# Kernel optimization log

Measured on AMD Instinct MI355X. Metric: run time of the kernel, lower is better.

The kernel has to match this reference:

```python
import jax, jax.numpy as jnp
import numpy as np

B, N, E = 32, 2048, 65536
SLOPE = 0.01  # torch LeakyReLU default

def _lrelu(x):
    return jax.nn.leaky_relu(x, SLOPE)

def setup_inputs() -> dict:
    key = jax.random.key(0)
    ks = jax.random.split(key, 32)
    def w(k, shape):
        return jax.random.normal(k, shape, dtype=jnp.float32) * 0.1
    inp = {}
    inp['vertices'] = jax.random.normal(ks[0], (B, N, 11), dtype=jnp.float32)
    inp['edges'] = jax.random.randint(ks[1], (2, E), 0, N, dtype=jnp.int32)
    # x/y/th pairwise feature extractors: Conv2d(1,8,kernel=(1,2)) == linear 2->8
    inp['Wx'], inp['bx'] = w(ks[2], (8, 2)), w(ks[3], (8,))
    inp['Wy'], inp['by'] = w(ks[4], (8, 2)), w(ks[5], (8,))
    inp['Wth'], inp['bth'] = w(ks[6], (8, 2)), w(ks[7], (8,))
    # config_lin: 24->32, 32->32 (1x1 convs)
    inp['W1c'], inp['b1c'] = w(ks[8], (32, 24)), w(ks[9], (32,))
    inp['W2c'], inp['b2c'] = w(ks[10], (32, 32)), w(ks[11], (32,))
    # vertex_lin: 64->32, 32->32
    inp['W1v'], inp['b1v'] = w(ks[12], (32, 64)), w(ks[13], (32,))
    inp['W2v'], inp['b2v'] = w(ks[14], (32, 32)), w(ks[15], (32,))
    # edge_lin: Conv2d(1,32,kernel=(68,1)) == linear 68->32, then 32->32
    inp['W1e'], inp['b1e'] = w(ks[16], (32, 68)), w(ks[17], (32,))
    inp['W2e'], inp['b2e'] = w(ks[18], (32, 32)), w(ks[19], (32,))
    # vertex_output_lin: Conv2d(1,32,kernel=(32,1)) == linear 32->32, then 32->1
    inp['W1o'], inp['b1o'] = w(ks[20], (32, 32)), w(ks[21], (32,))
    inp['W2o'], inp['b2o'] = w(ks[22], (1, 32)), w(ks[23], (1,))
    # graph_output_lin: Linear(N, 1)
    inp['Wg'], inp['bg'] = w(ks[24], (1, N)) * 0.1, w(ks[25], (1,))
    return inp

def _pair_feat(a, b, W, bb):
    # a, b: [B,N] -> [B,N,2] @ W.T -> [B,N,8]
    p = jnp.stack([a, b], axis=-1)
    return _lrelu(p @ W.T + bb)

def reference(vertices, edges, Wx, bx, Wy, by, Wth, bth, W1c, b1c, W2c, b2c,
              W1v, b1v, W2v, b2v, W1e, b1e, W2e, b2e, W1o, b1o, W2o, b2o, Wg, bg):
    qk = vertices[:, :, 0:3]
    q0 = vertices[:, :, 3:6]
    qg = vertices[:, :, 6:9]
    col = vertices[:, :, 9:11]  # [B,N,2]

    def config_feat(qa, qb):
        fx = _pair_feat(qa[..., 0], qb[..., 0], Wx, bx)
        fy = _pair_feat(qa[..., 1], qb[..., 1], Wy, by)
        fth = _pair_feat(qa[..., 2], qb[..., 2], Wth, bth)
        c = jnp.concatenate([fx, fy, fth], axis=-1)  # [B,N,24]
        h = _lrelu(c @ W1c.T + b1c)
        return _lrelu(h @ W2c.T + b2c)  # [B,N,32]

    cf = jnp.concatenate([config_feat(qk, q0), config_feat(qk, qg)], axis=-1)  # [B,N,64]
    vf = _lrelu(cf @ W1v.T + b1v)
    vf = _lrelu(vf @ W2v.T + b2v)  # [B,N,32]
    vf = jnp.concatenate([vf, col], axis=-1)  # [B,N,34]

    src, dst = edges[0], edges[1]
    pair = jnp.concatenate([vf[:, src, :], vf[:, dst, :]], axis=-1)  # [B,E,68]
    m = jax.nn.relu(pair @ W1e.T + b1e)
    m = _lrelu(m @ W2e.T + b2e)  # [B,E,32]

    n_nodes = vertices.shape[1]
    sums = jnp.zeros((vertices.shape[0], n_nodes, m.shape[-1]), m.dtype).at[:, dst, :].add(m)
    cnt = jnp.zeros((n_nodes,), m.dtype).at[dst].add(1.0)
    agg = sums / jnp.maximum(cnt, 1.0)[None, :, None]  # scatter_mean; empty bins -> 0

    fv = jax.nn.relu(agg @ W1o.T + b1o)
    fv = _lrelu(fv @ W2o.T + b2o)[..., 0]  # [B,N]
    return jax.nn.sigmoid(fv @ Wg.T + bg)  # [B,1]
```

## Files before the change

kernel.cpp:

```cpp
#include <hip/hip_runtime.h>
#include <math.h>

constexpr int B = 32;
constexpr int NN = 2048;
constexpr int E = 65536;
constexpr float SLOPE = 0.01f;

typedef __attribute__((ext_vector_type(8))) short bf16x8;
typedef __attribute__((ext_vector_type(4))) float f32x4;

__device__ __forceinline__ float lrelu(float x) { return fmaxf(x, SLOPE * x); }
__device__ __forceinline__ int imin(int a, int b) { return a < b ? a : b; }
__device__ __forceinline__ int imax(int a, int b) { return a > b ? a : b; }

__device__ __forceinline__ unsigned int cvtpk(float lo, float hi) {
    unsigned int r;
    asm("v_cvt_pk_bf16_f32 %0, %1, %2" : "=v"(r) : "v"(lo), "v"(hi));
    return r;
}

__device__ __forceinline__ void unpack_bf16(unsigned int u, float& lo, float& hi) {
    lo = __uint_as_float(u << 16);
    hi = __uint_as_float(u & 0xffff0000u);
}

__device__ __forceinline__ void unpack8(const uint4& u, float f[8]) {
    unpack_bf16(u.x, f[0], f[1]);
    unpack_bf16(u.y, f[2], f[3]);
    unpack_bf16(u.z, f[4], f[5]);
    unpack_bf16(u.w, f[6], f[7]);
}

union U8 { unsigned int u[4]; bf16x8 v; uint4 q; };

__device__ __forceinline__ void fma_grp16(const float* __restrict__ Wt, int jj, int o0,
                                          const uint4& r, float acc[16]) {
    float x[8]; unpack8(r, x);
    const float* Wp = Wt + jj * 256 + o0;
    #pragma unroll
    for (int jo = 0; jo < 8; ++jo) {
        #pragma unroll
        for (int o = 0; o < 16; ++o) acc[o] += x[jo] * Wp[jo * 32 + o];
    }
}

__device__ __forceinline__ void layerN16(const unsigned short* col, int G, int o0,
                                         const float* __restrict__ Wt, float acc[16]) {
    uint4 cur = *(const uint4*)col;
    #pragma unroll 1
    for (int jj = 0; jj < G; ++jj) {
        uint4 nxt = (jj + 1 < G) ? *(const uint4*)(col + (jj + 1) * 8) : cur;
        fma_grp16(Wt, jj, o0, cur, acc);
        cur = nxt;
    }
}

__device__ __forceinline__ void layer2N16(const unsigned short* col, int G, int o0,
                                          const float* __restrict__ Ws,
                                          const float* __restrict__ Wd,
                                          float a1[16], float a2[16]) {
    uint4 cur = *(const uint4*)col;
    #pragma unroll 1
    for (int jj = 0; jj < G; ++jj) {
        uint4 nxt = (jj + 1 < G) ? *(const uint4*)(col + (jj + 1) * 8) : cur;
        float x[8]; unpack8(cur, x);
        const float* Wps = Ws + jj * 256 + o0;
        const float* Wpd = Wd + jj * 256 + o0;
        #pragma unroll
        for (int jo = 0; jo < 8; ++jo) {
            #pragma unroll
            for (int o = 0; o < 16; ++o) a1[o] += x[jo] * Wps[jo * 32 + o];
            #pragma unroll
            for (int o = 0; o < 16; ++o) a2[o] += x[jo] * Wpd[jo * 32 + o];
        }
        cur = nxt;
    }
}

__global__ __launch_bounds__(256) void prep_zero_kernel(
    const float* __restrict__ W1c, const float* __restrict__ W2c,
    const float* __restrict__ W1v, const float* __restrict__ W2v,
    const float* __restrict__ W1e, const float* __restrict__ W2e,
    const float* __restrict__ W1o,
    float* __restrict__ W1cT, float* __restrict__ W2cT,
    float* __restrict__ W1vT, float* __restrict__ W2vT,
    float* __restrict__ W1sT, float* __restrict__ W1dT,
    unsigned short* __restrict__ W2eb, float* __restrict__ W1oT,
    int* __restrict__ cnt, int* __restrict__ cursor)
{
    int blk = blockIdx.x;
    if (blk < 8) {
        int i = blk * 256 + threadIdx.x;
        cnt[i] = 0;
        cursor[i] = 0;
        return;
    }
    int t = (blk - 8) * 256 + threadIdx.x;
    for (int i = t; i < 32 * 24; i += 1024) W1cT[(i % 24) * 32 + i / 24] = W1c[i];
    for (int i = t; i < 32 * 32; i += 1024) W2cT[(i % 32) * 32 + i / 32] = W2c[i];
    for (int i = t; i < 32 * 64; i += 1024) W1vT[(i % 64) * 32 + i / 64] = W1v[i];
    for (int i = t; i < 32 * 32; i += 1024) W2vT[(i % 32) * 32 + i / 32] = W2v[i];
    for (int i = t; i < 32 * 68; i += 1024) {
        int o = i / 68, j = i % 68;
        if (j < 34) W1sT[j * 32 + o] = W1e[i];
        else        W1dT[(j - 34) * 32 + o] = W1e[i];
    }
    for (int i = t; i < 32 * 32; i += 1024) {
        unsigned int u = __float_as_uint(W2e[i]);
        u += 0x7fffu + ((u >> 16) & 1u);
        W2eb[i] = (unsigned short)(u >> 16);
    }
    for (int i = t; i < 32 * 32; i += 1024) W1oT[(i % 32) * 32 + i / 32] = W1o[i];
}

__global__ __launch_bounds__(256) void count_kernel(const int* __restrict__ edges, int* __restrict__ cnt)
{
    int e = blockIdx.x * 256 + threadIdx.x;
    if (e < E) atomicAdd(&cnt[edges[E + e]], 1);
}

__global__ __launch_bounds__(1024) void scan_kernel(const int* __restrict__ cnt, int* __restrict__ offs)
{
    __shared__ int s[1024];
    int t = threadIdx.x;
    int c0 = cnt[2 * t], c1 = cnt[2 * t + 1];
    int own = c0 + c1;
    s[t] = own;
    __syncthreads();
    int v = own;
    for (int d = 1; d < 1024; d <<= 1) {
        int add = (t >= d) ? s[t - d] : 0;
        __syncthreads();
        v += add;
        s[t] = v;
        __syncthreads();
    }
    int excl = v - own;
    offs[2 * t] = excl;
    offs[2 * t + 1] = excl + c0;
    if (t == 1023) offs[2048] = v;
}

__global__ __launch_bounds__(256) void fill_kernel(
    const int* __restrict__ edges, const int* __restrict__ offs,
    int* __restrict__ cursor, int* __restrict__ elist)
{
    int e = blockIdx.x * 256 + threadIdx.x;
    if (e < E) {
        int d = edges[E + e];
        int p = atomicAdd(&cursor[d], 1);
        elist[offs[d] + p] = edges[e];
    }
}

__global__ __launch_bounds__(256) void vertex_kernel(
    const float* __restrict__ vert,
    const float* __restrict__ Wx,  const float* __restrict__ bx,
    const float* __restrict__ Wy,  const float* __restrict__ by,
    const float* __restrict__ Wth, const float* __restrict__ bth,
    const float* __restrict__ b1c, const float* __restrict__ b2c,
    const float* __restrict__ b1v, const float* __restrict__ b2v,
    const float* __restrict__ b1e,
    const float* __restrict__ W1cT, const float* __restrict__ W2cT,
    const float* __restrict__ W1vT, const float* __restrict__ W2vT,
    const float* __restrict__ W1sT, const float* __restrict__ W1dT,
    unsigned int* __restrict__ asrc, unsigned int* __restrict__ adst)
{
    __shared__ unsigned short bufS[128 * 40];
    __shared__ unsigned short bufT[128 * 40];
    __shared__ unsigned short bufC[128 * 72];
    int tid = threadIdx.x;
    int w = tid >> 6, lane = tid & 63;
    int g = w >> 1;
    int h = w & 1;
    int o0 = __builtin_amdgcn_readfirstlane(h << 4);
    int nl = g * 64 + lane;
    int idx = blockIdx.x * 128 + nl;
    unsigned short* Sc = bufS + nl * 40;
    unsigned short* Tc = bufT + nl * 40;
    unsigned short* Cc = bufC + nl * 72;

    const float* v = vert + (size_t)idx * 11;
    float qk0 = v[0], qk1 = v[1], qk2 = v[2];
    float q00 = v[3], q01 = v[4], q02 = v[5];
    float qg0 = v[6], qg1 = v[7], qg2 = v[8];
    float col0 = v[9], col1 = v[10];

    for (int cfh = 0; cfh < 2; ++cfh) {
        float a0 = cfh ? qg0 : q00;
        float a1 = cfh ? qg1 : q01;
        float a2 = cfh ? qg2 : q02;
        if (h == 0) {
            #pragma unroll
            for (int i = 0; i < 4; ++i) {
                ((unsigned int*)Sc)[i] = cvtpk(
                    lrelu(qk0 * Wx[4 * i]     + a0 * Wx[4 * i + 1] + bx[2 * i]),
                    lrelu(qk0 * Wx[4 * i + 2] + a0 * Wx[4 * i + 3] + bx[2 * i + 1]));
                ((unsigned int*)Sc)[4 + i] = cvtpk(
                    lrelu(qk1 * Wy[4 * i]     + a1 * Wy[4 * i + 1] + by[2 * i]),
                    lrelu(qk1 * Wy[4 * i + 2] + a1 * Wy[4 * i + 3] + by[2 * i + 1]));
            }
        } else {
            #pragma unroll
            for (int i = 0; i < 4; ++i) {
                ((unsigned int*)Sc)[8 + i] = cvtpk(
                    lrelu(qk2 * Wth[4 * i]     + a2 * Wth[4 * i + 1] + bth[2 * i]),
                    lrelu(qk2 * Wth[4 * i + 2] + a2 * Wth[4 * i + 3] + bth[2 * i + 1]));
            }
        }
        __syncthreads();

        float hh[16];
        #pragma unroll
        for (int o = 0; o < 16; ++o) hh[o] = b1c[o0 + o];
        layerN16(Sc, 3, o0, W1cT, hh);
        #pragma unroll
        for (int q = 0; q < 8; ++q)
            ((unsigned int*)Tc)[h * 8 + q] = cvtpk(lrelu(hh[2 * q]), lrelu(hh[2 * q + 1]));
        __syncthreads();

        float gg[16];
        #pragma unroll
        for (int o = 0; o < 16; ++o) gg[o] = b2c[o0 + o];
        layerN16(Tc, 4, o0, W2cT, gg);
        #pragma unroll
        for (int q = 0; q < 8; ++q)
            ((unsigned int*)Cc)[cfh * 16 + h * 8 + q] =
                cvtpk(lrelu(gg[2 * q]), lrelu(gg[2 * q + 1]));
        __syncthreads();
    }

    float v1[16];
    #pragma unroll
    for (int o = 0; o < 16; ++o) v1[o] = b1v[o0 + o];
    layerN16(Cc, 8, o0, W1vT, v1);
    #pragma unroll
    for (int q = 0; q < 8; ++q)
        ((unsigned int*)Sc)[h * 8 + q] = cvtpk(lrelu(v1[2 * q]), lrelu(v1[2 * q + 1]));
    __syncthreads();

    float v2[16];
    #pragma unroll
    for (int o = 0; o < 16; ++o) v2[o] = b2v[o0 + o];
    layerN16(Sc, 4, o0, W2vT, v2);
    #pragma unroll
    for (int q = 0; q < 8; ++q)
        ((unsigned int*)Tc)[h * 8 + q] = cvtpk(lrelu(v2[2 * q]), lrelu(v2[2 * q + 1]));
    __syncthreads();

    float as[16], ad[16];
    #pragma unroll
    for (int o = 0; o < 16; ++o) { as[o] = 0.f; ad[o] = b1e[o0 + o]; }
    layer2N16(Tc, 4, o0, W1sT, W1dT, as, ad);
    #pragma unroll
    for (int o = 0; o < 16; ++o) {
        as[o] += col0 * W1sT[32 * 32 + o0 + o] + col1 * W1sT[33 * 32 + o0 + o];
        ad[o] += col0 * W1dT[32 * 32 + o0 + o] + col1 * W1dT[33 * 32 + o0 + o];
    }

    unsigned int* ps = asrc + ((size_t)idx << 4) + h * 8;
    unsigned int* pd = adst + ((size_t)idx << 4) + h * 8;
    #pragma unroll
    for (int q = 0; q < 8; ++q) {
        ps[q] = cvtpk(as[2 * q], as[2 * q + 1]);
        pd[q] = cvtpk(ad[2 * q], ad[2 * q + 1]);
    }
}

__device__ __forceinline__ void chunk_step(
    const uint4* __restrict__ abq, const int* __restrict__ elist,
    int e0, int end, int e1, int col, int grp,
    uint4& su_c, int& src_n, const float adr[8],
    const U8& Bf0, const U8& Bf1, float bias0, float bias1,
    float& s0, float& s1)
{
    uint4 su_n = abq[(src_n << 2) | grp];
    int src_n2 = elist[imin(e0 + 32 + col, e1)];

    float h0, h1, h2, h3, h4, h5, h6, h7;
    {
        float lo, hi;
        unpack_bf16(su_c.x, lo, hi);
        h0 = fmaxf(lo + adr[0], 0.f); h1 = fmaxf(hi + adr[1], 0.f);
        unpack_bf16(su_c.y, lo, hi);
        h2 = fmaxf(lo + adr[2], 0.f); h3 = fmaxf(hi + adr[3], 0.f);
        unpack_bf16(su_c.z, lo, hi);
        h4 = fmaxf(lo + adr[4], 0.f); h5 = fmaxf(hi + adr[5], 0.f);
        unpack_bf16(su_c.w, lo, hi);
        h6 = fmaxf(lo + adr[6], 0.f); h7 = fmaxf(hi + adr[7], 0.f);
    }
    U8 A;
    A.u[0] = cvtpk(h0, h1);
    A.u[1] = cvtpk(h2, h3);
    A.u[2] = cvtpk(h4, h5);
    A.u[3] = cvtpk(h6, h7);
    if ((e0 + col) >= end) {
        A.u[0] = 0; A.u[1] = 0; A.u[2] = 0; A.u[3] = 0;
    }

    f32x4 acc0 = {bias0, bias0, bias0, bias0};
    f32x4 acc1 = {bias1, bias1, bias1, bias1};
    acc0 = __builtin_amdgcn_mfma_f32_16x16x32_bf16(A.v, Bf0.v, acc0, 0, 0, 0);
    acc1 = __builtin_amdgcn_mfma_f32_16x16x32_bf16(A.v, Bf1.v, acc1, 0, 0, 0);

    #pragma unroll
    for (int r = 0; r < 4; ++r) {
        s0 += lrelu(acc0[r]);
        s1 += lrelu(acc1[r]);
    }
    su_c = su_n;
    src_n = src_n2;
}

__global__ __launch_bounds__(1024) void edge_kernel(
    const unsigned int* __restrict__ asrc, const unsigned int* __restrict__ adst,
    const int* __restrict__ elist, const int* __restrict__ offs,
    const unsigned short* __restrict__ W2eb, const float* __restrict__ b2e,
    const float* __restrict__ W1oT, const float* __restrict__ b1o,
    const float* __restrict__ W2o,  const float* __restrict__ b2o,
    float* __restrict__ fv)
{
    int logical = (blockIdx.x & 7) * 64 + (blockIdx.x >> 3);
    int b = logical >> 4;
    int seg = logical & 15;
    int tid = threadIdx.x;
    int wv = tid >> 6;
    int lane = tid & 63;
    int col = lane & 15;
    int grp = lane >> 4;

    const uint4* abq = (const uint4*)(asrc + (((size_t)b * NN) << 4));

    U8 Bf0, Bf1;
    Bf0.q = *(const uint4*)(W2eb + col * 32 + grp * 8);
    Bf1.q = *(const uint4*)(W2eb + (col + 16) * 32 + grp * 8);
    float bias0 = b2e[col];
    float bias1 = b2e[col + 16];
    float lb0 = lrelu(bias0);
    float lb1 = lrelu(bias1);
    int o = lane & 31;
    float w2oc = W2o[o];
    float b1oc = b1o[o];
    float b2oc = b2o[0];
    float w1or[32];
    #pragma unroll
    for (int j = 0; j < 32; ++j) w1or[j] = W1oT[j * 32 + o];
    const unsigned int* adb = adst + (((size_t)b * NN) << 4) + grp * 4;

    int dbase = seg * 128 + wv * 8;
    for (int dp = 0; dp < 4; ++dp) {
        int dA = dbase + 2 * dp;
        int dB = dA + 1;
        int startA = offs[dA];
        int endA = offs[dB];
        int endB = offs[dB + 1];
        int startB = endA;
        int degA = endA - startA;
        int degB = endB - startB;
        int e1A = imax(endA - 1, 0);
        int e1B = imax(endB - 1, 0);

        const uint4 duA = *(const uint4*)(adb + ((size_t)dA << 4));
        const uint4 duB = *(const uint4*)(adb + ((size_t)dB << 4));
        float adrA[8]; unpack8(duA, adrA);
        float adrB[8]; unpack8(duB, adrB);

        int n = imax((degA + 15) >> 4, (degB + 15) >> 4);

        float s0A = 0.f, s1A = 0.f, s0B = 0.f, s1B = 0.f;
        if (n > 0) {
            int srcA = elist[imin(startA + col, e1A)];
            int srcB = elist[imin(startB + col, e1B)];
            uint4 suA = abq[(srcA << 2) | grp];
            uint4 suB = abq[(srcB << 2) | grp];
            int srcnA = elist[imin(startA + 16 + col, e1A)];
            int srcnB = elist[imin(startB + 16 + col, e1B)];

            for (int it = 0; it < n; ++it) {
                int e0A = startA + (it << 4);
                int e0B = startB + (it << 4);
                chunk_step(abq, elist, e0A, endA, e1A, col, grp,
                           suA, srcnA, adrA, Bf0, Bf1, bias0, bias1, s0A, s1A);
                chunk_step(abq, elist, e0B, endB, e1B, col, grp,
                           suB, srcnB, adrB, Bf0, Bf1, bias0, bias1, s0B, s1B);
            }
        }

        s0A += __shfl_xor(s0A, 16); s0A += __shfl_xor(s0A, 32);
        s1A += __shfl_xor(s1A, 16); s1A += __shfl_xor(s1A, 32);
        s0B += __shfl_xor(s0B, 16); s0B += __shfl_xor(s0B, 32);
        s1B += __shfl_xor(s1B, 16); s1B += __shfl_xor(s1B, 32);

        float padA = (float)(16 * n - degA);
        float padB = (float)(16 * n - degB);
        s0A -= padA * lb0; s1A -= padA * lb1;
        s0B -= padB * lb0; s1B -= padB * lb1;

        float invA = 1.f / fmaxf((float)degA, 1.f);
        float invB = 1.f / fmaxf((float)degB, 1.f);
        float a0A = s0A * invA, a1A = s1A * invA;
        float a0B = s0B * invB, a1B = s1B * invB;

        float pA[4] = {b1oc, 0.f, 0.f, 0.f};
        float pB[4] = {b1oc, 0.f, 0.f, 0.f};
        #pragma unroll
        for (int j = 0; j < 16; ++j) {
            pA[j & 3] += __shfl(a0A, j) * w1or[j];
            pA[j & 3] += __shfl(a1A, j) * w1or[16 + j];
            pB[j & 3] += __shfl(a0B, j) * w1or[j];
            pB[j & 3] += __shfl(a1B, j) * w1or[16 + j];
        }
        float f1A = (pA[0] + pA[1]) + (pA[2] + pA[3]);
        float f1B = (pB[0] + pB[1]) + (pB[2] + pB[3]);

        float tA = fmaxf(f1A, 0.f) * w2oc;
        float tB = fmaxf(f1B, 0.f) * w2oc;
        tA += __shfl_xor(tA, 1);  tB += __shfl_xor(tB, 1);
        tA += __shfl_xor(tA, 2);  tB += __shfl_xor(tB, 2);
        tA += __shfl_xor(tA, 4);  tB += __shfl_xor(tB, 4);
        tA += __shfl_xor(tA, 8);  tB += __shfl_xor(tB, 8);
        tA += __shfl_xor(tA, 16); tB += __shfl_xor(tB, 16);
        if (lane == 0) {
            fv[(size_t)b * NN + dA] = lrelu(tA + b2oc);
            fv[(size_t)b * NN + dB] = lrelu(tB + b2oc);
        }
    }
}

__global__ __launch_bounds__(256) void final_kernel(
    const float* __restrict__ fv, const float* __restrict__ Wg,
    const float* __restrict__ bg, float* __restrict__ out)
{
    int b = blockIdx.x;
    int t = threadIdx.x;
    float p = 0.f;
    for (int n = t; n < NN; n += 256) p += fv[(size_t)b * NN + n] * Wg[n];
    __shared__ float red[256];
    red[t] = p;
    __syncthreads();
    for (int s = 128; s > 0; s >>= 1) {
        if (t < s) red[t] += red[t + s];
        __syncthreads();
    }
    if (t == 0) {
        float x = red[0] + bg[0];
        out[b] = 1.f / (1.f + expf(-x));
    }
}

extern "C" void kernel_launch(void* const* d_in, const int* in_sizes, int n_in,
                              void* d_out, int out_size, void* d_ws, size_t ws_size,
                              hipStream_t stream)
{
    const float* vert = (const float*)d_in[0];
    const int*   edges = (const int*)d_in[1];
    const float* Wx  = (const float*)d_in[2];
    const float* bx  = (const float*)d_in[3];
    const float* Wy  = (const float*)d_in[4];
    const float* by  = (const float*)d_in[5];
    const float* Wth = (const float*)d_in[6];
    const float* bth = (const float*)d_in[7];
    const float* W1c = (const float*)d_in[8];
    const float* b1c = (const float*)d_in[9];
    const float* W2c = (const float*)d_in[10];
    const float* b2c = (const float*)d_in[11];
    const float* W1v = (const float*)d_in[12];
    const float* b1v = (const float*)d_in[13];
    const float* W2v = (const float*)d_in[14];
    const float* b2v = (const float*)d_in[15];
    const float* W1e = (const float*)d_in[16];
    const float* b1e = (const float*)d_in[17];
    const float* W2e = (const float*)d_in[18];
    const float* b2e = (const float*)d_in[19];
    const float* W1o = (const float*)d_in[20];
    const float* b1o = (const float*)d_in[21];
    const float* W2o = (const float*)d_in[22];
    const float* b2o = (const float*)d_in[23];
    const float* Wg  = (const float*)d_in[24];
    const float* bg  = (const float*)d_in[25];
    float* out = (float*)d_out;

    char* w = (char*)d_ws;
    unsigned int* asrc = (unsigned int*)w; w += (size_t)B * NN * 32 * 2;
    unsigned int* adst = (unsigned int*)w; w += (size_t)B * NN * 32 * 2;
    float* fv   = (float*)w; w += (size_t)B * NN * 4;
    float* W1cT = (float*)w; w += 32 * 24 * 4;
    float* W2cT = (float*)w; w += 32 * 32 * 4;
    float* W1vT = (float*)w; w += 32 * 64 * 4;
    float* W2vT = (float*)w; w += 32 * 32 * 4;
    float* W1sT = (float*)w; w += 34 * 32 * 4;
    float* W1dT = (float*)w; w += 34 * 32 * 4;
    float* W1oT = (float*)w; w += 32 * 32 * 4;
    unsigned short* W2eb = (unsigned short*)w; w += 32 * 32 * 2;
    int* cnt    = (int*)w;   w += NN * 4;
    int* cursor = (int*)w;   w += NN * 4;
    int* offs   = (int*)w;   w += 2052 * 4;
    int* elist  = (int*)w;   w += E * 4;

    prep_zero_kernel<<<12, 256, 0, stream>>>(W1c, W2c, W1v, W2v, W1e, W2e, W1o,
                                             W1cT, W2cT, W1vT, W2vT, W1sT, W1dT,
                                             W2eb, W1oT, cnt, cursor);
    count_kernel<<<E / 256, 256, 0, stream>>>(edges, cnt);
    scan_kernel<<<1, 1024, 0, stream>>>(cnt, offs);
    fill_kernel<<<E / 256, 256, 0, stream>>>(edges, offs, cursor, elist);

    vertex_kernel<<<(B * NN) / 128, 256, 0, stream>>>(
        vert, Wx, bx, Wy, by, Wth, bth, b1c, b2c, b1v, b2v, b1e,
        W1cT, W2cT, W1vT, W2vT, W1sT, W1dT, asrc, adst);

    edge_kernel<<<B * 16, 1024, 0, stream>>>(
        asrc, adst, elist, offs, W2eb, b2e, W1oT, b1o, W2o, b2o, fv);

    final_kernel<<<B, 256, 0, stream>>>(fv, Wg, bg, out);
}
```

Baseline: 110.5 us.

## Batch vertex output layer into bf16 MFMA and halve edge-kernel block size

Replaces the per-destination shuffle-based 32x32 output matmul with a per-wave batch of 16 aggregated node rows staged in LDS as bf16, followed by one pair of MFMA ops. W1o is converted to bf16 in the prep kernel. Blocks shrink from 1024 to 512 threads, so each wave now handles 16 destinations instead of 8. This removes the 32 register-held weights and the many shuffles per node, at the cost of bf16 rounding on the aggregated features and less parallelism per block.

Result: faster. 101.0 us (-8.6%).

```diff
diff --git a/kernel.cpp b/kernel.cpp
--- a/kernel.cpp
+++ b/kernel.cpp
@@ -85,7 +85,7 @@
     float* __restrict__ W1cT, float* __restrict__ W2cT,
     float* __restrict__ W1vT, float* __restrict__ W2vT,
     float* __restrict__ W1sT, float* __restrict__ W1dT,
-    unsigned short* __restrict__ W2eb, float* __restrict__ W1oT,
+    unsigned short* __restrict__ W2eb, unsigned short* __restrict__ W1oTb,
     int* __restrict__ cnt, int* __restrict__ cursor)
 {
     int blk = blockIdx.x;
@@ -110,7 +110,15 @@
         u += 0x7fffu + ((u >> 16) & 1u);
         W2eb[i] = (unsigned short)(u >> 16);
     }
-    for (int i = t; i < 32 * 32; i += 1024) W1oT[(i % 32) * 32 + i / 32] = W1o[i];
+    for (int i = t; i < 512; i += 1024) {
+        int o = i >> 4, m = i & 15;
+        unsigned int u0 = __float_as_uint(W1o[o * 32 + m]);
+        u0 += 0x7fffu + ((u0 >> 16) & 1u);
+        unsigned int u1 = __float_as_uint(W1o[o * 32 + 16 + m]);
+        u1 += 0x7fffu + ((u1 >> 16) & 1u);
+        W1oTb[o * 32 + 2 * m]     = (unsigned short)(u0 >> 16);
+        W1oTb[o * 32 + 2 * m + 1] = (unsigned short)(u1 >> 16);
+    }
 }
 
 __global__ __launch_bounds__(256) void count_kernel(const int* __restrict__ edges, int* __restrict__ cnt)
@@ -312,14 +320,15 @@
     src_n = src_n2;
 }
 
-__global__ __launch_bounds__(1024) void edge_kernel(
+__global__ __launch_bounds__(512) void edge_kernel(
     const unsigned int* __restrict__ asrc, const unsigned int* __restrict__ adst,
     const int* __restrict__ elist, const int* __restrict__ offs,
     const unsigned short* __restrict__ W2eb, const float* __restrict__ b2e,
-    const float* __restrict__ W1oT, const float* __restrict__ b1o,
+    const unsigned short* __restrict__ W1oTb, const float* __restrict__ b1o,
     const float* __restrict__ W2o,  const float* __restrict__ b2o,
     float* __restrict__ fv)
 {
+    __shared__ unsigned int aggbuf[8 * 16 * 20];
     int logical = (blockIdx.x & 7) * 64 + (blockIdx.x >> 3);
     int b = logical >> 4;
     int seg = logical & 15;
@@ -330,25 +339,27 @@
     int grp = lane >> 4;
 
     const uint4* abq = (const uint4*)(asrc + (((size_t)b * NN) << 4));
+    unsigned int* wvagg = aggbuf + wv * (16 * 20);
 
     U8 Bf0, Bf1;
     Bf0.q = *(const uint4*)(W2eb + col * 32 + grp * 8);
     Bf1.q = *(const uint4*)(W2eb + (col + 16) * 32 + grp * 8);
+    U8 Bo0, Bo1;
+    Bo0.q = *(const uint4*)(W1oTb + col * 32 + grp * 8);
+    Bo1.q = *(const uint4*)(W1oTb + (col + 16) * 32 + grp * 8);
     float bias0 = b2e[col];
     float bias1 = b2e[col + 16];
     float lb0 = lrelu(bias0);
     float lb1 = lrelu(bias1);
-    int o = lane & 31;
-    float w2oc = W2o[o];
-    float b1oc = b1o[o];
+    float b1o_lo = b1o[col];
+    float b1o_hi = b1o[col + 16];
+    float w2o_lo = W2o[col];
+    float w2o_hi = W2o[col + 16];
     float b2oc = b2o[0];
-    float w1or[32];
-    #pragma unroll
-    for (int j = 0; j < 32; ++j) w1or[j] = W1oT[j * 32 + o];
     const unsigned int* adb = adst + (((size_t)b * NN) << 4) + grp * 4;
 
-    int dbase = seg * 128 + wv * 8;
-    for (int dp = 0; dp < 4; ++dp) {
+    int dbase = seg * 128 + wv * 16;
+    for (int dp = 0; dp < 8; ++dp) {
         int dA = dbase + 2 * dp;
         int dB = dA + 1;
         int startA = offs[dA];
@@ -398,32 +409,28 @@
 
         float invA = 1.f / fmaxf((float)degA, 1.f);
         float invB = 1.f / fmaxf((float)degB, 1.f);
-        float a0A = s0A * invA, a1A = s1A * invA;
-        float a0B = s0B * invB, a1B = s1B * invB;
-
-        float pA[4] = {b1oc, 0.f, 0.f, 0.f};
-        float pB[4] = {b1oc, 0.f, 0.f, 0.f};
-        #pragma unroll
-        for (int j = 0; j < 16; ++j) {
-            pA[j & 3] += __shfl(a0A, j) * w1or[j];
-            pA[j & 3] += __shfl(a1A, j) * w1or[16 + j];
-            pB[j & 3] += __shfl(a0B, j) * w1or[j];
-            pB[j & 3] += __shfl(a1B, j) * w1or[16 + j];
+        if (grp == 0) {
+            wvagg[(2 * dp) * 20 + col]     = cvtpk(s0A * invA, s1A * invA);
+            wvagg[(2 * dp + 1) * 20 + col] = cvtpk(s0B * invB, s1B * invB);
         }
-        float f1A = (pA[0] + pA[1]) + (pA[2] + pA[3]);
-        float f1B = (pB[0] + pB[1]) + (pB[2] + pB[3]);
-
-        float tA = fmaxf(f1A, 0.f) * w2oc;
-        float tB = fmaxf(f1B, 0.f) * w2oc;
-        tA += __shfl_xor(tA, 1);  tB += __shfl_xor(tB, 1);
-        tA += __shfl_xor(tA, 2);  tB += __shfl_xor(tB, 2);
-        tA += __shfl_xor(tA, 4);  tB += __shfl_xor(tB, 4);
-        tA += __shfl_xor(tA, 8);  tB += __shfl_xor(tB, 8);
-        tA += __shfl_xor(tA, 16); tB += __shfl_xor(tB, 16);
-        if (lane == 0) {
-            fv[(size_t)b * NN + dA] = lrelu(tA + b2oc);
-            fv[(size_t)b * NN + dB] = lrelu(tB + b2oc);
-        }
+    }
+
+    U8 Ao;
+    Ao.q = *(const uint4*)(wvagg + col * 20 + grp * 4);
+    f32x4 acc0 = {b1o_lo, b1o_lo, b1o_lo, b1o_lo};
+    f32x4 acc1 = {b1o_hi, b1o_hi, b1o_hi, b1o_hi};
+    acc0 = __builtin_amdgcn_mfma_f32_16x16x32_bf16(Ao.v, Bo0.v, acc0, 0, 0, 0);
+    acc1 = __builtin_amdgcn_mfma_f32_16x16x32_bf16(Ao.v, Bo1.v, acc1, 0, 0, 0);
+
+    float* fvb = fv + (size_t)b * NN + dbase + grp * 4;
+    #pragma unroll
+    for (int r = 0; r < 4; ++r) {
+        float t = fmaxf(acc0[r], 0.f) * w2o_lo + fmaxf(acc1[r], 0.f) * w2o_hi;
+        t += __shfl_xor(t, 1);
+        t += __shfl_xor(t, 2);
+        t += __shfl_xor(t, 4);
+        t += __shfl_xor(t, 8);
+        if (col == 0) fvb[r] = lrelu(t + b2oc);
     }
 }
 
@@ -490,8 +497,8 @@
     float* W2vT = (float*)w; w += 32 * 32 * 4;
     float* W1sT = (float*)w; w += 34 * 32 * 4;
     float* W1dT = (float*)w; w += 34 * 32 * 4;
-    float* W1oT = (float*)w; w += 32 * 32 * 4;
-    unsigned short* W2eb = (unsigned short*)w; w += 32 * 32 * 2;
+    unsigned short* W2eb  = (unsigned short*)w; w += 32 * 32 * 2;
+    unsigned short* W1oTb = (unsigned short*)w; w += 32 * 32 * 2;
     int* cnt    = (int*)w;   w += NN * 4;
     int* cursor = (int*)w;   w += NN * 4;
     int* offs   = (int*)w;   w += 2052 * 4;
@@ -499,7 +506,7 @@
 
     prep_zero_kernel<<<12, 256, 0, stream>>>(W1c, W2c, W1v, W2v, W1e, W2e, W1o,
                                              W1cT, W2cT, W1vT, W2vT, W1sT, W1dT,
-                                             W2eb, W1oT, cnt, cursor);
+                                             W2eb, W1oTb, cnt, cursor);
     count_kernel<<<E / 256, 256, 0, stream>>>(edges, cnt);
     scan_kernel<<<1, 1024, 0, stream>>>(cnt, offs);
     fill_kernel<<<E / 256, 256, 0, stream>>>(edges, offs, cursor, elist);
@@ -508,8 +515,8 @@
         vert, Wx, bx, Wy, by, Wth, bth, b1c, b2c, b1v, b2v, b1e,
         W1cT, W2cT, W1vT, W2vT, W1sT, W1dT, asrc, adst);
 
-    edge_kernel<<<B * 16, 1024, 0, stream>>>(
-        asrc, adst, elist, offs, W2eb, b2e, W1oT, b1o, W2o, b2o, fv);
+    edge_kernel<<<B * 16, 512, 0, stream>>>(
+        asrc, adst, elist, offs, W2eb, b2e, W1oTb, b1o, W2o, b2o, fv);
 
     final_kernel<<<B, 256, 0, stream>>>(fv, Wg, bg, out);
 }
```
